# Optimization experiments

Hardware: AMD Instinct MI355X
Metric: run time of the kernel (lower is better)

## Reference

```python
import jax, jax.numpy as jnp
import numpy as np

K = 10
ALPHA = 0.1
BETA = 0.9
GAMMA = BETA ** K + ALPHA * sum(BETA ** i for i in range(K))


def setup_inputs() -> dict:
    key = jax.random.key(0)
    k1, k2, k3 = jax.random.split(key, 3)
    N, D, E = 100000, 256, 1600000
    x = jax.random.normal(k1, (N, D), dtype=jnp.float32)
    edge_weight = jax.random.uniform(k2, (E,), dtype=jnp.float32)
    edge_index = jax.random.randint(k3, (2, E), 0, N, dtype=jnp.int32)
    return {"x": x, "edge_weight": edge_weight, "edge_index": edge_index}


def reference(x, edge_weight, edge_index):
    N = x.shape[0]
    # gcn_norm_adj with renorm: add self-loops (weight 1) then D^-1/2 A D^-1/2
    loops = jnp.arange(N, dtype=edge_index.dtype)
    row = jnp.concatenate([edge_index[0], loops])
    col = jnp.concatenate([edge_index[1], loops])
    w = jnp.concatenate([edge_weight, jnp.ones((N,), dtype=x.dtype)])
    deg = jax.ops.segment_sum(w, row, num_segments=N)
    dinv = jnp.where(deg > 0, jax.lax.rsqrt(deg), 0.0)
    wn = dinv[row] * w * dinv[col]  # normalized edge weights [E+N]

    h = x
    out = h
    for _ in range(K):
        # SpMM: out[r] = sum_e wn[e] * out[col[e]] for row[e]==r
        msg = wn[:, None] * out[col]
        out = jax.ops.segment_sum(msg, row, num_segments=N)
        out = out * BETA + h * ALPHA
    out = out / GAMMA
    return out
```

## Files before the change

### kernel.cpp

```cpp
#include <hip/hip_runtime.h>
#include <hip/hip_fp16.h>
#include <math.h>

#define DFEAT 256
#define KITER 10
#define ALPHA 0.1f
#define BETA 0.9f
#define SCAN_CHUNK 2048

#define WSCALE 268435456.0
#define CNT_SHIFT 40


__global__ void edge_pass1_kernel(const int* __restrict__ row,
                                  const float* __restrict__ w,
                                  unsigned long long* __restrict__ pk,
                                  int* __restrict__ rank, int E) {
    int e = blockIdx.x * 256 + threadIdx.x;
    if (e < E) {
        int r = row[e];
        unsigned long long add = (1ULL << CNT_SHIFT) |
            (unsigned long long)((double)w[e] * WSCALE);
        unsigned long long old = atomicAdd(&pk[r], add);
        rank[e] = (int)(old >> CNT_SHIFT);
    }
}

__global__ void dinv_kernel(const unsigned long long* __restrict__ pk,
                            float* __restrict__ dinv, int n) {
    int i = blockIdx.x * 256 + threadIdx.x;
    if (i < n) {
        unsigned long long v = pk[i];
        float deg = (float)((double)(v & ((1ULL << CNT_SHIFT) - 1)) * (1.0 / WSCALE));
        dinv[i] = rsqrtf(deg + 1.0f);
    }
}


__global__ __launch_bounds__(256) void scan1_kernel(const unsigned long long* __restrict__ pk,
                                                    int* __restrict__ row_ptr,
                                                    int* __restrict__ partial, int n) {
    __shared__ int wsum[4];
    int b = blockIdx.x;
    int base = b * SCAN_CHUNK;
    int tid = threadIdx.x;
    int lane = tid & 63, wv = tid >> 6;

    int v[8];
    int s = 0;
    #pragma unroll
    for (int j = 0; j < 8; ++j) {
        int i = base + tid * 8 + j;
        v[j] = (i < n) ? (int)(pk[i] >> CNT_SHIFT) : 0;
        s += v[j];
    }
    int incl = s;
    #pragma unroll
    for (int off = 1; off < 64; off <<= 1) {
        int t = __shfl_up(incl, off, 64);
        if (lane >= off) incl += t;
    }
    if (lane == 63) wsum[wv] = incl;
    __syncthreads();
    int woff = 0;
    for (int w = 0; w < wv; ++w) woff += wsum[w];
    int run = woff + incl - s;
    #pragma unroll
    for (int j = 0; j < 8; ++j) {
        int i = base + tid * 8 + j;
        if (i < n) row_ptr[i] = run;
        run += v[j];
    }
    if (tid == 255) partial[b] = run;
}

__global__ void scan2_kernel(int* __restrict__ partial, int nb) {
    __shared__ int tmp[1024];
    int tid = threadIdx.x;
    int v = (tid < nb) ? partial[tid] : 0;
    tmp[tid] = v;
    __syncthreads();
    for (int off = 1; off < 1024; off <<= 1) {
        int t = (tid >= off) ? tmp[tid - off] : 0;
        __syncthreads();
        tmp[tid] += t;
        __syncthreads();
    }
    if (tid < nb) partial[tid] = tmp[tid] - v;
}

__global__ void scan3_kernel(int* __restrict__ row_ptr,
                             const int* __restrict__ partial, int n, int E) {
    int i = blockIdx.x * 256 + threadIdx.x;
    if (i < n) {
        row_ptr[i] += partial[i / SCAN_CHUNK];
    } else if (i == n) {
        row_ptr[n] = E;
    }
}

__global__ void scatter_kernel(const int* __restrict__ row, const int* __restrict__ col,
                               const float* __restrict__ w, const int* __restrict__ rank,
                               const int* __restrict__ row_ptr,
                               int2* __restrict__ cw, int E) {
    int e = blockIdx.x * 256 + threadIdx.x;
    if (e < E) {
        int r = row[e];
        int pos = row_ptr[r] + rank[e];
        cw[pos] = make_int2(col[e], __float_as_int(w[e]));
    }
}

__global__ void xprime_kernel(const float* __restrict__ x, const float* __restrict__ dinv,
                              __half* __restrict__ dst, size_t n4) {
    size_t i = (size_t)blockIdx.x * 256 + threadIdx.x;
    if (i < n4) {
        float4 v = ((const float4*)x)[i];
        float dr = dinv[i >> 6];
        __half2 h0 = __floats2half2_rn(dr * v.x, dr * v.y);
        __half2 h1 = __floats2half2_rn(dr * v.z, dr * v.w);
        float2 o;
        o.x = *reinterpret_cast<float*>(&h0);
        o.y = *reinterpret_cast<float*>(&h1);
        ((float2*)dst)[i] = o;
    }
}

#define ACC(g, wbits) { float wv = __int_as_float(wbits); \
    __half2 h0_ = *reinterpret_cast<__half2*>(&g.x); \
    __half2 h1_ = *reinterpret_cast<__half2*>(&g.y); \
    float2 u0_ = __half22float2(h0_); float2 u1_ = __half22float2(h1_); \
    a0 += wv * u0_.x; a1 += wv * u0_.y; a2 += wv * u1_.x; a3 += wv * u1_.y; }

template<int FINAL>
__global__ __launch_bounds__(256) void spmm_h_kernel(
        const __half* __restrict__ in, const __half* __restrict__ xh,
        float* __restrict__ outf, __half* __restrict__ outh,
        const int* __restrict__ row_ptr, const int2* __restrict__ cw,
        const float* __restrict__ dinv,
        int n, float inv_gamma) {
    int wave = threadIdx.x >> 6;
    int lane = threadIdx.x & 63;
    int r = blockIdx.x * 4 + wave;
    if (r >= n) return;

    int start = row_ptr[r];
    int end   = row_ptr[r + 1];
    float dr  = dinv[r];
    float c1  = BETA * dr * dr;

    float2 xraw = ((const float2*)(xh + (size_t)r * DFEAT))[lane];

    float2 sraw = ((const float2*)(in + (size_t)r * DFEAT))[lane];
    __half2 s0 = *reinterpret_cast<__half2*>(&sraw.x);
    __half2 s1 = *reinterpret_cast<__half2*>(&sraw.y);
    float2 sf0 = __half22float2(s0), sf1 = __half22float2(s1);
    float a0 = sf0.x, a1 = sf0.y, a2 = sf1.x, a3 = sf1.y;

    int e = start;
    for (; e + 4 <= end; e += 4) {
        int2 p0 = cw[e];
        int2 p1 = cw[e + 1];
        int2 p2 = cw[e + 2];
        int2 p3 = cw[e + 3];
        float2 g0 = ((const float2*)(in + (size_t)p0.x * DFEAT))[lane];
        float2 g1 = ((const float2*)(in + (size_t)p1.x * DFEAT))[lane];
        float2 g2 = ((const float2*)(in + (size_t)p2.x * DFEAT))[lane];
        float2 g3 = ((const float2*)(in + (size_t)p3.x * DFEAT))[lane];
        ACC(g0, p0.y);
        ACC(g1, p1.y);
        ACC(g2, p2.y);
        ACC(g3, p3.y);
    }
    for (; e < end; ++e) {
        int2 p = cw[e];
        float2 g = ((const float2*)(in + (size_t)p.x * DFEAT))[lane];
        ACC(g, p.y);
    }

    __half2 x0 = *reinterpret_cast<__half2*>(&xraw.x);
    __half2 x1 = *reinterpret_cast<__half2*>(&xraw.y);
    float2 xf0 = __half22float2(x0), xf1 = __half22float2(x1);
    float o0 = c1 * a0 + ALPHA * xf0.x;
    float o1 = c1 * a1 + ALPHA * xf0.y;
    float o2 = c1 * a2 + ALPHA * xf1.x;
    float o3 = c1 * a3 + ALPHA * xf1.y;

    if (FINAL) {
        float up = inv_gamma / dr;
        ((float4*)(outf + (size_t)r * DFEAT))[lane] =
            make_float4(o0 * up, o1 * up, o2 * up, o3 * up);
    } else {
        __half2 h0 = __floats2half2_rn(o0, o1);
        __half2 h1 = __floats2half2_rn(o2, o3);
        float2 o;
        o.x = *reinterpret_cast<float*>(&h0);
        o.y = *reinterpret_cast<float*>(&h1);
        ((float2*)(outh + (size_t)r * DFEAT))[lane] = o;
    }
}


extern "C" void kernel_launch(void* const* d_in, const int* in_sizes, int n_in,
                              void* d_out, int out_size, void* d_ws, size_t ws_size,
                              hipStream_t stream) {
    const float* x  = (const float*)d_in[0];
    const float* ew = (const float*)d_in[1];
    const int*   ei = (const int*)d_in[2];
    int n = in_sizes[0] / DFEAT;
    int E = in_sizes[1];
    const int* row = ei;
    const int* col = ei + E;
    float* out = (float*)d_out;

    char* ws = (char*)d_ws;
    auto alloc = [&](size_t bytes) {
        char* p = ws;
        ws += (bytes + 255) & ~(size_t)255;
        return p;
    };
    unsigned long long* pk = (unsigned long long*)alloc((size_t)n * 8);
    int*    rank    = (int*)  alloc((size_t)E * 4);
    int*    row_ptr = (int*)  alloc((size_t)(n + 1) * 4);
    int*    partial = (int*)  alloc((size_t)1024 * 4);
    float*  dinv    = (float*)alloc((size_t)n * 4);
    int2*   cw      = (int2*) alloc((size_t)E * 8);
    __half* xh      = (__half*)alloc((size_t)n * DFEAT * 2);
    __half* H0      = (__half*)alloc((size_t)n * DFEAT * 2);
    __half* H1      = (__half*)d_out;

    hipMemsetAsync(pk, 0, (size_t)n * 8, stream);

    edge_pass1_kernel<<<(E + 255) / 256, 256, 0, stream>>>(row, ew, pk, rank, E);
    dinv_kernel<<<(n + 255) / 256, 256, 0, stream>>>(pk, dinv, n);

    int nb = (n + SCAN_CHUNK - 1) / SCAN_CHUNK;
    scan1_kernel<<<nb, 256, 0, stream>>>(pk, row_ptr, partial, n);
    scan2_kernel<<<1, 1024, 0, stream>>>(partial, nb);
    scan3_kernel<<<(n + 256) / 256, 256, 0, stream>>>(row_ptr, partial, n, E);

    scatter_kernel<<<(E + 255) / 256, 256, 0, stream>>>(row, col, ew, rank, row_ptr, cw, E);

    size_t n4 = (size_t)n * DFEAT / 4;
    xprime_kernel<<<(int)((n4 + 255) / 256), 256, 0, stream>>>(x, dinv, xh, n4);

    double gamma = pow((double)BETA, KITER);
    for (int i = 0; i < KITER; ++i) gamma += (double)ALPHA * pow((double)BETA, i);
    float inv_gamma = (float)(1.0 / gamma);

    int grid = (n + 3) / 4;
    const __half* cur = xh;
    __half* bufs[2] = { H0, H1 };
    for (int k = 0; k < KITER; ++k) {
        if (k < KITER - 1) {
            __half* o = bufs[k & 1];
            spmm_h_kernel<0><<<grid, 256, 0, stream>>>(cur, xh, nullptr, o,
                                                       row_ptr, cw, dinv, n, 1.0f);
            cur = o;
        } else {
            spmm_h_kernel<1><<<grid, 256, 0, stream>>>(cur, xh, out, nullptr,
                                                       row_ptr, cw, dinv, n, inv_gamma);
        }
    }
}
```

Baseline: 1.447 ms.

## Slice SpMM into feature chunks with column-bucketed, packed 32-bit edges

Splits each row's 256-wide feature vector into 8 slices of 32 halves, each handled by its own block, with 16 lanes-groups striding over edges and a shuffle reduction at the end. Edges within a row are ordered by column bucket (col>>15) using packed 7-bit per-bucket counters in the degree atomic. Each edge becomes a 32-bit word holding a 17-bit column and a truncated fp16 weight, halving edge traffic. The aim is better cache locality for gathers within a slice and less index bandwidth. In exchange, edge metadata is re-read once per slice, a cross-lane reduction is added, and the weights lose precision. The packing also assumes N fits in 17 bits and that no row has more than 127 edges in any one bucket.

```diff
diff --git a/kernel.cpp b/kernel.cpp
--- a/kernel.cpp
+++ b/kernel.cpp
@@ -7,37 +7,39 @@
 #define ALPHA 0.1f
 #define BETA 0.9f
 #define SCAN_CHUNK 2048
+#define BUCKET_SHIFT 15
 
 #define WSCALE 268435456.0
-#define CNT_SHIFT 40
-
-
-__global__ void edge_pass1_kernel(const int* __restrict__ row,
-                                  const float* __restrict__ w,
-                                  unsigned long long* __restrict__ pk,
-                                  int* __restrict__ rank, int E) {
+#define WSUM_MASK ((1ULL << 34) - 1)
+
+typedef float f32x4 __attribute__((ext_vector_type(4)));
+typedef unsigned u32;
+typedef unsigned long long u64;
+
+
+__global__ void pass1_kernel(const int* __restrict__ row, const int* __restrict__ col,
+                             const float* __restrict__ w,
+                             u64* __restrict__ pk, u32* __restrict__ rankA, int E) {
     int e = blockIdx.x * 256 + threadIdx.x;
     if (e < E) {
         int r = row[e];
-        unsigned long long add = (1ULL << CNT_SHIFT) |
-            (unsigned long long)((double)w[e] * WSCALE);
-        unsigned long long old = atomicAdd(&pk[r], add);
-        rank[e] = (int)(old >> CNT_SHIFT);
-    }
-}
-
-__global__ void dinv_kernel(const unsigned long long* __restrict__ pk,
-                            float* __restrict__ dinv, int n) {
+        u32 b = ((u32)col[e]) >> BUCKET_SHIFT;
+        u64 add = (u64)((double)w[e] * WSCALE) | (1ULL << (34 + 7 * b));
+        u64 old = atomicAdd(&pk[r], add);
+        rankA[e] = (u32)((old >> (34 + 7 * b)) & 0x7F);
+    }
+}
+
+__global__ void dinv_kernel(const u64* __restrict__ pk, float* __restrict__ dinv, int n) {
     int i = blockIdx.x * 256 + threadIdx.x;
     if (i < n) {
-        unsigned long long v = pk[i];
-        float deg = (float)((double)(v & ((1ULL << CNT_SHIFT) - 1)) * (1.0 / WSCALE));
+        float deg = (float)((double)(pk[i] & WSUM_MASK) * (1.0 / WSCALE));
         dinv[i] = rsqrtf(deg + 1.0f);
     }
 }
 
 
-__global__ __launch_bounds__(256) void scan1_kernel(const unsigned long long* __restrict__ pk,
+__global__ __launch_bounds__(256) void scan1_kernel(const u64* __restrict__ pk,
                                                     int* __restrict__ row_ptr,
                                                     int* __restrict__ partial, int n) {
     __shared__ int wsum[4];
@@ -51,8 +53,14 @@
     #pragma unroll
     for (int j = 0; j < 8; ++j) {
         int i = base + tid * 8 + j;
-        v[j] = (i < n) ? (int)(pk[i] >> CNT_SHIFT) : 0;
-        s += v[j];
+        int cnt = 0;
+        if (i < n) {
+            u64 q = pk[i];
+            cnt = (int)(((q >> 34) & 0x7F) + ((q >> 41) & 0x7F) +
+                        ((q >> 48) & 0x7F) + ((q >> 55) & 0x7F));
+        }
+        v[j] = cnt;
+        s += cnt;
     }
     int incl = s;
     #pragma unroll
@@ -100,14 +108,22 @@
 }
 
 __global__ void scatter_kernel(const int* __restrict__ row, const int* __restrict__ col,
-                               const float* __restrict__ w, const int* __restrict__ rank,
-                               const int* __restrict__ row_ptr,
-                               int2* __restrict__ cw, int E) {
+                               const float* __restrict__ w, const u32* __restrict__ rankA,
+                               const u64* __restrict__ pk, const int* __restrict__ row_ptr,
+                               u32* __restrict__ cwp, int E) {
     int e = blockIdx.x * 256 + threadIdx.x;
     if (e < E) {
         int r = row[e];
-        int pos = row_ptr[r] + rank[e];
-        cw[pos] = make_int2(col[e], __float_as_int(w[e]));
+        u32 c = (u32)col[e];
+        u32 b = c >> BUCKET_SHIFT;
+        u64 v = pk[r];
+        u32 c0 = (u32)((v >> 34) & 0x7F);
+        u32 c1 = (u32)((v >> 41) & 0x7F);
+        u32 c2 = (u32)((v >> 48) & 0x7F);
+        u32 off = (b > 0 ? c0 : 0) + (b > 1 ? c1 : 0) + (b > 2 ? c2 : 0);
+        u32 pos = (u32)row_ptr[r] + off + rankA[e];
+        u32 wb = (u32)__half_as_ushort(__float2half_rn(w[e])) & 0xFFFEu;
+        cwp[pos] = (wb << 16) | c;
     }
 }
 
@@ -126,77 +142,99 @@
     }
 }
 
-#define ACC(g, wbits) { float wv = __int_as_float(wbits); \
-    __half2 h0_ = *reinterpret_cast<__half2*>(&g.x); \
-    __half2 h1_ = *reinterpret_cast<__half2*>(&g.y); \
-    float2 u0_ = __half22float2(h0_); float2 u1_ = __half22float2(h1_); \
-    a0 += wv * u0_.x; a1 += wv * u0_.y; a2 += wv * u1_.x; a3 += wv * u1_.y; }
-
 template<int FINAL>
-__global__ __launch_bounds__(256) void spmm_h_kernel(
+__global__ __launch_bounds__(256) void spmm_slice_kernel(
         const __half* __restrict__ in, const __half* __restrict__ xh,
         float* __restrict__ outf, __half* __restrict__ outh,
-        const int* __restrict__ row_ptr, const int2* __restrict__ cw,
-        const float* __restrict__ dinv,
-        int n, float inv_gamma) {
+        const int* __restrict__ row_ptr, const u32* __restrict__ cwp,
+        const float* __restrict__ dinv, int n, float inv_gamma) {
     int wave = threadIdx.x >> 6;
     int lane = threadIdx.x & 63;
-    int r = blockIdx.x * 4 + wave;
+    u32 s = (u32)blockIdx.x & 7u;
+    int r = (blockIdx.x >> 3) * 4 + wave;
     if (r >= n) return;
 
     int start = row_ptr[r];
     int end   = row_ptr[r + 1];
-    float dr  = dinv[r];
-    float c1  = BETA * dr * dr;
-
-    float2 xraw = ((const float2*)(xh + (size_t)r * DFEAT))[lane];
-
-    float2 sraw = ((const float2*)(in + (size_t)r * DFEAT))[lane];
-    __half2 s0 = *reinterpret_cast<__half2*>(&sraw.x);
-    __half2 s1 = *reinterpret_cast<__half2*>(&sraw.y);
-    float2 sf0 = __half22float2(s0), sf1 = __half22float2(s1);
-    float a0 = sf0.x, a1 = sf0.y, a2 = sf1.x, a3 = sf1.y;
-
-    int e = start;
-    for (; e + 4 <= end; e += 4) {
-        int2 p0 = cw[e];
-        int2 p1 = cw[e + 1];
-        int2 p2 = cw[e + 2];
-        int2 p3 = cw[e + 3];
-        float2 g0 = ((const float2*)(in + (size_t)p0.x * DFEAT))[lane];
-        float2 g1 = ((const float2*)(in + (size_t)p1.x * DFEAT))[lane];
-        float2 g2 = ((const float2*)(in + (size_t)p2.x * DFEAT))[lane];
-        float2 g3 = ((const float2*)(in + (size_t)p3.x * DFEAT))[lane];
-        ACC(g0, p0.y);
-        ACC(g1, p1.y);
-        ACC(g2, p2.y);
-        ACC(g3, p3.y);
-    }
-    for (; e < end; ++e) {
-        int2 p = cw[e];
-        float2 g = ((const float2*)(in + (size_t)p.x * DFEAT))[lane];
-        ACC(g, p.y);
-    }
-
-    __half2 x0 = *reinterpret_cast<__half2*>(&xraw.x);
-    __half2 x1 = *reinterpret_cast<__half2*>(&xraw.y);
-    float2 xf0 = __half22float2(x0), xf1 = __half22float2(x1);
-    float o0 = c1 * a0 + ALPHA * xf0.x;
-    float o1 = c1 * a1 + ALPHA * xf0.y;
-    float o2 = c1 * a2 + ALPHA * xf1.x;
-    float o3 = c1 * a3 + ALPHA * xf1.y;
-
-    if (FINAL) {
-        float up = inv_gamma / dr;
-        ((float4*)(outf + (size_t)r * DFEAT))[lane] =
-            make_float4(o0 * up, o1 * up, o2 * up, o3 * up);
-    } else {
-        __half2 h0 = __floats2half2_rn(o0, o1);
-        __half2 h1 = __floats2half2_rn(o2, o3);
-        float2 o;
-        o.x = *reinterpret_cast<float*>(&h0);
-        o.y = *reinterpret_cast<float*>(&h1);
-        ((float2*)(outh + (size_t)r * DFEAT))[lane] = o;
+    int g   = lane >> 2;
+    int sub = lane & 3;
+
+    float a00 = 0.f, a01 = 0.f, a10 = 0.f, a11 = 0.f;
+    float a20 = 0.f, a21 = 0.f, a30 = 0.f, a31 = 0.f;
+
+    const __half* sbase = in + (s << 5) + (sub << 3);
+    for (int e = start + g; e < end; e += 16) {
+        u32 p = __builtin_nontemporal_load(cwp + e);
+        u32 c = p & 0x1FFFFu;
+        float wf = __half2float(__ushort_as_half((unsigned short)((p >> 16) & 0xFFFEu)));
+        f32x4 v = *(const f32x4*)(sbase + ((size_t)c << 8));
+        __half2* hv = (__half2*)&v;
+        float2 f0 = __half22float2(hv[0]);
+        float2 f1 = __half22float2(hv[1]);
+        float2 f2 = __half22float2(hv[2]);
+        float2 f3 = __half22float2(hv[3]);
+        a00 += wf * f0.x; a01 += wf * f0.y;
+        a10 += wf * f1.x; a11 += wf * f1.y;
+        a20 += wf * f2.x; a21 += wf * f2.y;
+        a30 += wf * f3.x; a31 += wf * f3.y;
+    }
+
+    #pragma unroll
+    for (int m = 4; m < 64; m <<= 1) {
+        a00 += __shfl_xor(a00, m, 64);
+        a01 += __shfl_xor(a01, m, 64);
+        a10 += __shfl_xor(a10, m, 64);
+        a11 += __shfl_xor(a11, m, 64);
+        a20 += __shfl_xor(a20, m, 64);
+        a21 += __shfl_xor(a21, m, 64);
+        a30 += __shfl_xor(a30, m, 64);
+        a31 += __shfl_xor(a31, m, 64);
+    }
+
+    if (g == 0) {
+        size_t off = ((size_t)r << 8) + (s << 5) + (sub << 3);
+        float dr = dinv[r];
+        float c1v = BETA * dr * dr;
+
+        f32x4 sv = *(const f32x4*)(in + off);
+        __half2* sh = (__half2*)&sv;
+        float2 s0 = __half22float2(sh[0]);
+        float2 s1 = __half22float2(sh[1]);
+        float2 s2 = __half22float2(sh[2]);
+        float2 s3 = __half22float2(sh[3]);
+
+        f32x4 xv = __builtin_nontemporal_load((const f32x4*)(xh + off));
+        __half2* xp = (__half2*)&xv;
+        float2 x0 = __half22float2(xp[0]);
+        float2 x1 = __half22float2(xp[1]);
+        float2 x2 = __half22float2(xp[2]);
+        float2 x3 = __half22float2(xp[3]);
+
+        float o00 = c1v * (a00 + s0.x) + ALPHA * x0.x;
+        float o01 = c1v * (a01 + s0.y) + ALPHA * x0.y;
+        float o10 = c1v * (a10 + s1.x) + ALPHA * x1.x;
+        float o11 = c1v * (a11 + s1.y) + ALPHA * x1.y;
+        float o20 = c1v * (a20 + s2.x) + ALPHA * x2.x;
+        float o21 = c1v * (a21 + s2.y) + ALPHA * x2.y;
+        float o30 = c1v * (a30 + s3.x) + ALPHA * x3.x;
+        float o31 = c1v * (a31 + s3.y) + ALPHA * x3.y;
+
+        if (FINAL) {
+            float up = inv_gamma / dr;
+            float* op = outf + off;
+            f32x4 w0 = { o00 * up, o01 * up, o10 * up, o11 * up };
+            f32x4 w1 = { o20 * up, o21 * up, o30 * up, o31 * up };
+            __builtin_nontemporal_store(w0, (f32x4*)op);
+            __builtin_nontemporal_store(w1, (f32x4*)(op + 4));
+        } else {
+            f32x4 ov;
+            __half2* oh = (__half2*)&ov;
+            oh[0] = __floats2half2_rn(o00, o01);
+            oh[1] = __floats2half2_rn(o10, o11);
+            oh[2] = __floats2half2_rn(o20, o21);
+            oh[3] = __floats2half2_rn(o30, o31);
+            __builtin_nontemporal_store(ov, (f32x4*)(outh + off));
+        }
     }
 }
 
@@ -219,19 +257,19 @@
         ws += (bytes + 255) & ~(size_t)255;
         return p;
     };
-    unsigned long long* pk = (unsigned long long*)alloc((size_t)n * 8);
-    int*    rank    = (int*)  alloc((size_t)E * 4);
+    u64*    pk      = (u64*)  alloc((size_t)n * 8);
+    u32*    rankA   = (u32*)  alloc((size_t)E * 4);
     int*    row_ptr = (int*)  alloc((size_t)(n + 1) * 4);
     int*    partial = (int*)  alloc((size_t)1024 * 4);
     float*  dinv    = (float*)alloc((size_t)n * 4);
-    int2*   cw      = (int2*) alloc((size_t)E * 8);
+    u32*    cwp     = (u32*)  alloc((size_t)E * 4);
     __half* xh      = (__half*)alloc((size_t)n * DFEAT * 2);
     __half* H0      = (__half*)alloc((size_t)n * DFEAT * 2);
     __half* H1      = (__half*)d_out;
 
     hipMemsetAsync(pk, 0, (size_t)n * 8, stream);
 
-    edge_pass1_kernel<<<(E + 255) / 256, 256, 0, stream>>>(row, ew, pk, rank, E);
+    pass1_kernel<<<(E + 255) / 256, 256, 0, stream>>>(row, col, ew, pk, rankA, E);
     dinv_kernel<<<(n + 255) / 256, 256, 0, stream>>>(pk, dinv, n);
 
     int nb = (n + SCAN_CHUNK - 1) / SCAN_CHUNK;
@@ -239,7 +277,8 @@
     scan2_kernel<<<1, 1024, 0, stream>>>(partial, nb);
     scan3_kernel<<<(n + 256) / 256, 256, 0, stream>>>(row_ptr, partial, n, E);
 
-    scatter_kernel<<<(E + 255) / 256, 256, 0, stream>>>(row, col, ew, rank, row_ptr, cw, E);
+    scatter_kernel<<<(E + 255) / 256, 256, 0, stream>>>(row, col, ew, rankA, pk,
+                                                        row_ptr, cwp, E);
 
     size_t n4 = (size_t)n * DFEAT / 4;
     xprime_kernel<<<(int)((n4 + 255) / 256), 256, 0, stream>>>(x, dinv, xh, n4);
@@ -248,18 +287,18 @@
     for (int i = 0; i < KITER; ++i) gamma += (double)ALPHA * pow((double)BETA, i);
     float inv_gamma = (float)(1.0 / gamma);
 
-    int grid = (n + 3) / 4;
+    int grid = 8 * ((n + 3) / 4);
     const __half* cur = xh;
     __half* bufs[2] = { H0, H1 };
     for (int k = 0; k < KITER; ++k) {
         if (k < KITER - 1) {
             __half* o = bufs[k & 1];
-            spmm_h_kernel<0><<<grid, 256, 0, stream>>>(cur, xh, nullptr, o,
-                                                       row_ptr, cw, dinv, n, 1.0f);
+            spmm_slice_kernel<0><<<grid, 256, 0, stream>>>(cur, xh, nullptr, o,
+                                                           row_ptr, cwp, dinv, n, 1.0f);
             cur = o;
         } else {
-            spmm_h_kernel<1><<<grid, 256, 0, stream>>>(cur, xh, out, nullptr,
-                                                       row_ptr, cw, dinv, n, inv_gamma);
+            spmm_slice_kernel<1><<<grid, 256, 0, stream>>>(cur, xh, out, nullptr,
+                                                           row_ptr, cwp, dinv, n, inv_gamma);
         }
     }
 }
```

Result: slower. 3.757 ms (+159.6%).
